# Kernel tuning notes

Hardware: AMD Instinct MI355X
Metric: run time of the kernel (lower is better)

The kernel has to match this reference:

```python
import jax, jax.numpy as jnp
import numpy as np

DIM = 1024
NUM_HEADS = 16
HEAD_DIM = DIM // NUM_HEADS
SCALE = HEAD_DIM ** -0.5


def setup_inputs() -> dict:
    key = jax.random.key(0)
    ks = jax.random.split(key, 7)
    B, N, L, C = 2, 1024, 4096, DIM
    s = C ** -0.5
    return {
        "x": jax.random.normal(ks[0], (B, N, C), jnp.float32),
        "y": jax.random.normal(ks[1], (B, L, C), jnp.float32),
        "Wq": jax.random.normal(ks[2], (C, C), jnp.float32) * s,
        "Wk": jax.random.normal(ks[3], (C, C), jnp.float32) * s,
        "Wv": jax.random.normal(ks[4], (C, C), jnp.float32) * s,
        "Wp": jax.random.normal(ks[5], (C, C), jnp.float32) * s,
        "bp": jax.random.normal(ks[6], (C,), jnp.float32) * 0.01,
    }


def reference(x, y, Wq, Wk, Wv, Wp, bp):
    B, N, C = x.shape
    L = y.shape[1]
    H, D = NUM_HEADS, HEAD_DIM
    # torch nn.Linear: out = inp @ W.T
    q = (x @ Wq.T).reshape(B, N, H, D)
    k = (y @ Wk.T).reshape(B, L, H, D)
    v = (y @ Wv.T).reshape(B, L, H, D)
    attn = jnp.einsum("bnhd,blhd->bhnl", q, k)  # [B,H,N,L]
    attn = jax.nn.softmax(SCALE * attn, axis=-1)
    out = jnp.einsum("bhnl,blhd->bnhd", attn, v).reshape(B, N, C)
    return out @ Wp.T + bp
```

## Files before the change

### kernel.cpp

```cpp
#include <hip/hip_runtime.h>
#include <hip/hip_bf16.h>
#include <stdint.h>

typedef __bf16 bf16x8 __attribute__((ext_vector_type(8)));
typedef float f32x4 __attribute__((ext_vector_type(4)));

#define MFMA16(a, b, c) __builtin_amdgcn_mfma_f32_16x16x32_bf16((a), (b), (c), 0, 0, 0)

__device__ __forceinline__ ushort f2bf(float f) {
  union { float f; uint32_t u; } a; a.f = f;
  uint32_t u = a.u;
  return (ushort)((u + 0x7fffu + ((u >> 16) & 1u)) >> 16);
}

__device__ __forceinline__ void glds16(const void* g, void* l) {
  __builtin_amdgcn_global_load_lds(
      (const __attribute__((address_space(1))) uint32_t*)g,
      (__attribute__((address_space(3))) uint32_t*)l, 16, 0, 0);
}

__global__ __launch_bounds__(256) void cvt_xy(const float* __restrict__ x,
                                              const float* __restrict__ y,
                                              ushort* __restrict__ xb,
                                              ushort* __restrict__ yb) {
  const int bid = blockIdx.x;
  const float* in;
  ushort* out;
  int i;
  if (bid < 2048) { in = x; out = xb; i = bid * 1024 + threadIdx.x * 4; }
  else            { in = y; out = yb; i = (bid - 2048) * 1024 + threadIdx.x * 4; }
  float4 v = *(const float4*)(in + i);
  ushort4 o;
  o.x = f2bf(v.x); o.y = f2bf(v.y); o.z = f2bf(v.z); o.w = f2bf(v.w);
  *(ushort4*)(out + i) = o;
}

__global__ __launch_bounds__(256) void cvt_w(
    const float* __restrict__ a, const float* __restrict__ b,
    const float* __restrict__ c, const float* __restrict__ d,
    ushort* __restrict__ oa, ushort* __restrict__ ob,
    ushort* __restrict__ oc, ushort* __restrict__ od) {
  const int bid = blockIdx.x;
  const int sel = bid >> 10;
  const int i = (bid & 1023) * 1024 + threadIdx.x * 4;
  const float* in = (sel == 0) ? a : (sel == 1) ? b : (sel == 2) ? c : d;
  ushort* out = (sel == 0) ? oa : (sel == 1) ? ob : (sel == 2) ? oc : od;
  float4 v = *(const float4*)(in + i);
  ushort4 o;
  o.x = f2bf(v.x); o.y = f2bf(v.y); o.z = f2bf(v.z); o.w = f2bf(v.w);
  *(ushort4*)(out + i) = o;
}

template <int EPI, int BM>
__global__ __launch_bounds__(256) void gemm_bt(
    const ushort* __restrict__ A, const ushort* __restrict__ Bw,
    void* __restrict__ Cout, int K, float scale, const float* __restrict__ bias) {
  constexpr int NN = 1024;
  constexpr int WM = BM / 2;
  constexpr int AM = WM / 16;
  __shared__ ushort ldsA[BM * 32];
  __shared__ ushort ldsB[128 * 32];
  __shared__ ushort ldsT[(EPI == 1) ? (4 * 64 * 64) : 8];

  const int tid = threadIdx.x;
  const int w = tid >> 6, l = tid & 63;
  const int wm = w >> 1, wn = w & 1;
  const int m0 = blockIdx.x * BM, n0 = blockIdx.y * 128;

  f32x4 acc[AM][4] = {};

  const int srow = l >> 2;
  const int schunk = l & 3;

  for (int kt = 0; kt < K; kt += 32) {
#pragma unroll
    for (int r = 0; r < BM / 64; ++r) {
      const int rb = r * 64 + w * 16;
      const int row = rb + srow;
      const int j = schunk ^ ((row >> 1) & 3);
      glds16(A + (size_t)(m0 + row) * K + kt + j * 8, (char*)ldsA + rb * 64);
    }
#pragma unroll
    for (int r = 0; r < 2; ++r) {
      const int rb = r * 64 + w * 16;
      const int row = rb + srow;
      const int j = schunk ^ ((row >> 1) & 3);
      glds16(Bw + (size_t)(n0 + row) * K + kt + j * 8, (char*)ldsB + rb * 64);
    }
    __syncthreads();
    bf16x8 af[AM], bfr[4];
#pragma unroll
    for (int t = 0; t < AM; ++t) {
      const int rt = wm * WM + t * 16 + (l & 15);
      const int j = (l >> 4) ^ ((rt >> 1) & 3);
      af[t] = *(const bf16x8*)((const char*)ldsA + rt * 64 + j * 16);
    }
#pragma unroll
    for (int t = 0; t < 4; ++t) {
      const int rt = wn * 64 + t * 16 + (l & 15);
      const int j = (l >> 4) ^ ((rt >> 1) & 3);
      bfr[t] = *(const bf16x8*)((const char*)ldsB + rt * 64 + j * 16);
    }
#pragma unroll
    for (int am = 0; am < AM; ++am)
#pragma unroll
      for (int bn = 0; bn < 4; ++bn)
        acc[am][bn] = MFMA16(af[am], bfr[bn], acc[am][bn]);
    __syncthreads();
  }

  if constexpr (EPI == 0) {
#pragma unroll
    for (int am = 0; am < AM; ++am)
#pragma unroll
      for (int bn = 0; bn < 4; ++bn)
#pragma unroll
        for (int i = 0; i < 4; ++i) {
          const int row = m0 + wm * WM + am * 16 + (l >> 4) * 4 + i;
          const int col = n0 + wn * 64 + bn * 16 + (l & 15);
          ((ushort*)Cout)[(size_t)row * NN + col] = f2bf(acc[am][bn][i] * scale);
        }
  } else if constexpr (EPI == 2) {
#pragma unroll
    for (int am = 0; am < AM; ++am)
#pragma unroll
      for (int bn = 0; bn < 4; ++bn)
#pragma unroll
        for (int i = 0; i < 4; ++i) {
          const int row = m0 + wm * WM + am * 16 + (l >> 4) * 4 + i;
          const int col = n0 + wn * 64 + bn * 16 + (l & 15);
          ((float*)Cout)[(size_t)row * NN + col] = acc[am][bn][i] + bias[col];
        }
  } else {
    ushort* tp = ldsT + w * 4096;
#pragma unroll
    for (int am = 0; am < AM; ++am)
#pragma unroll
      for (int bn = 0; bn < 4; ++bn)
#pragma unroll
        for (int i = 0; i < 4; ++i) {
          const int ml = am * 16 + (l >> 4) * 4 + i;
          const int cl = bn * 16 + (l & 15);
          tp[cl * 64 + ml] = f2bf(acc[am][bn][i]);
        }
    __syncthreads();
#pragma unroll
    for (int it = 0; it < 8; ++it) {
      const int cl = it * 8 + (l >> 3);
      const int mc = l & 7;
      bf16x8 vv = *(const bf16x8*)(tp + cl * 64 + mc * 8);
      const int gcol = n0 + wn * 64 + cl;
      const int gm = m0 + wm * WM + mc * 8;
      const int b = gm >> 12;
      const int l_ = gm & 4095;
      const int h = gcol >> 6, d = gcol & 63;
      *(bf16x8*)((ushort*)Cout + (((size_t)b * 16 + h) * 64 + d) * 4096 + l_) = vv;
    }
  }
}

__global__ __launch_bounds__(256) void attn_fused(
    const ushort* __restrict__ qb, const ushort* __restrict__ kb,
    const ushort* __restrict__ vT, ushort* __restrict__ ao) {
  constexpr int H = 16, D = 64, L = 4096, N = 1024, KB = 128;
  __shared__ ushort ldsK[2][KB * 64];
  __shared__ ushort ldsV[2][64 * KB];
  __shared__ ushort ldsP[4 * 16 * KB];

  const int tid = threadIdx.x, w = tid >> 6, l = tid & 63;
  const int wg = blockIdx.x;
  const int v = (wg & 7) * 64 + (wg >> 3);
  const int bh = v >> 4;
  const int n0 = (v & 15) * 64;
  const int b = bh >> 4, h = bh & 15;

  bf16x8 qf[2];
  {
    const int qrow = n0 + w * 16 + (l & 15);
    const ushort* qp = qb + (((size_t)b * N + qrow) * H + h) * D + (l >> 4) * 8;
    qf[0] = *(const bf16x8*)qp;
    qf[1] = *(const bf16x8*)(qp + 32);
  }

  f32x4 oacc[4] = {};
  float m_run[4], l_run[4];
#pragma unroll
  for (int i = 0; i < 4; ++i) { m_run[i] = -1e30f; l_run[i] = 0.f; }

  auto stage = [&](int buf, int l0) {
#pragma unroll
    for (int r = 0; r < 4; ++r) {
      const int rb = (w * 4 + r) * 8;
      const int row = rb + (l >> 3);
      const int j = (l & 7) ^ (row & 7);
      glds16(kb + (((size_t)b * L + l0 + row) * H + h) * D + j * 8,
             (char*)ldsK[buf] + rb * 128);
    }
#pragma unroll
    for (int r = 0; r < 4; ++r) {
      const int rb = (w * 4 + r) * 4;
      const int row = rb + (l >> 4);
      const int j = (l & 15) ^ (row & 15);
      glds16(vT + ((size_t)(b * H + h) * D + row) * L + l0 + j * 8,
             (char*)ldsV[buf] + rb * 256);
    }
  };

  stage(0, 0);

  for (int t = 0; t < L / KB; ++t) {
    const int buf = t & 1;
    if (t < L / KB - 1) {
      stage(buf ^ 1, (t + 1) * KB);
      asm volatile("s_waitcnt vmcnt(8)" ::: "memory");
    } else {
      asm volatile("s_waitcnt vmcnt(0)" ::: "memory");
    }
    __builtin_amdgcn_sched_barrier(0);
    __builtin_amdgcn_s_barrier();
    __builtin_amdgcn_sched_barrier(0);

    f32x4 sacc[8] = {};
#pragma unroll
    for (int c = 0; c < 8; ++c) {
      const int rt = c * 16 + (l & 15);
#pragma unroll
      for (int ks = 0; ks < 2; ++ks) {
        const int j = ks * 4 + (l >> 4);
        bf16x8 kf = *(const bf16x8*)((const char*)ldsK[buf] + rt * 128 + ((j ^ (rt & 7)) << 4));
        sacc[c] = MFMA16(qf[ks], kf, sacc[c]);
      }
    }

    float corr[4];
#pragma unroll
    for (int i = 0; i < 4; ++i) {
      float mt = sacc[0][i];
#pragma unroll
      for (int c = 1; c < 8; ++c) mt = fmaxf(mt, sacc[c][i]);
#pragma unroll
      for (int dd = 1; dd < 16; dd <<= 1) mt = fmaxf(mt, __shfl_xor(mt, dd, 64));
      const float mn = fmaxf(m_run[i], mt);
      corr[i] = __builtin_amdgcn_exp2f(m_run[i] - mn);
      float rs = 0.f;
#pragma unroll
      for (int c = 0; c < 8; ++c) {
        const float p = __builtin_amdgcn_exp2f(sacc[c][i] - mn);
        sacc[c][i] = p;
        rs += p;
      }
#pragma unroll
      for (int dd = 1; dd < 16; dd <<= 1) rs += __shfl_xor(rs, dd, 64);
      l_run[i] = l_run[i] * corr[i] + rs;
      m_run[i] = mn;
    }
#pragma unroll
    for (int c = 0; c < 4; ++c)
#pragma unroll
      for (int i = 0; i < 4; ++i) oacc[c][i] *= corr[i];

    ushort* pp = ldsP + w * 2048;
#pragma unroll
    for (int c = 0; c < 8; ++c)
#pragma unroll
      for (int i = 0; i < 4; ++i) {
        const int row = (l >> 4) * 4 + i;
        const int col = c * 16 + (l & 15);
        *(ushort*)((char*)pp + row * 256 + (((col >> 3) ^ row) << 4) + ((col & 7) << 1)) =
            f2bf(sacc[c][i]);
      }
    asm volatile("s_waitcnt lgkmcnt(0)" ::: "memory");
    __builtin_amdgcn_sched_barrier(0);

    bf16x8 pf[4];
#pragma unroll
    for (int ks = 0; ks < 4; ++ks) {
      const int rt = l & 15;
      const int j = ks * 4 + (l >> 4);
      pf[ks] = *(const bf16x8*)((const char*)pp + rt * 256 + ((j ^ rt) << 4));
    }
#pragma unroll
    for (int c = 0; c < 4; ++c) {
      const int rt = c * 16 + (l & 15);
#pragma unroll
      for (int ks = 0; ks < 4; ++ks) {
        const int j = ks * 4 + (l >> 4);
        bf16x8 vf = *(const bf16x8*)((const char*)ldsV[buf] + rt * 256 + ((j ^ (rt & 15)) << 4));
        oacc[c] = MFMA16(pf[ks], vf, oacc[c]);
      }
    }
    __builtin_amdgcn_sched_barrier(0);
    __builtin_amdgcn_s_barrier();
    __builtin_amdgcn_sched_barrier(0);
  }

#pragma unroll
  for (int c = 0; c < 4; ++c)
#pragma unroll
    for (int i = 0; i < 4; ++i) {
      const int n = n0 + w * 16 + (l >> 4) * 4 + i;
      const int d = c * 16 + (l & 15);
      ao[(((size_t)b * N + n) * H + h) * D + d] = f2bf(oacc[c][i] / l_run[i]);
    }
}

extern "C" void kernel_launch(void* const* d_in, const int* in_sizes, int n_in,
                              void* d_out, int out_size, void* d_ws, size_t ws_size,
                              hipStream_t stream) {
  const float* x  = (const float*)d_in[0];
  const float* y  = (const float*)d_in[1];
  const float* Wq = (const float*)d_in[2];
  const float* Wk = (const float*)d_in[3];
  const float* Wv = (const float*)d_in[4];
  const float* Wp = (const float*)d_in[5];
  const float* bp = (const float*)d_in[6];
  float* out = (float*)d_out;

  const size_t M1 = 1u << 20;
  ushort* wsb = (ushort*)d_ws;
  ushort* xb  = wsb;
  ushort* yb  = wsb + 2 * M1;
  ushort* wqb = wsb + 10 * M1;
  ushort* wkb = wsb + 11 * M1;
  ushort* wvb = wsb + 12 * M1;
  ushort* wpb = wsb + 13 * M1;
  ushort* qbf = wsb + 14 * M1;
  ushort* kbf = wsb + 16 * M1;
  ushort* vtb = wsb + 24 * M1;
  ushort* aob = wsb + 32 * M1;

  cvt_xy<<<10240, 256, 0, stream>>>(x, y, xb, yb);
  cvt_w<<<4096, 256, 0, stream>>>(Wq, Wk, Wv, Wp, wqb, wkb, wvb, wpb);

  const float qscale = 0.125f * 1.4426950408889634f;
  gemm_bt<0, 64><<<dim3(32, 8), 256, 0, stream>>>(xb, wqb, qbf, 1024, qscale, nullptr);
  gemm_bt<0, 128><<<dim3(64, 8), 256, 0, stream>>>(yb, wkb, kbf, 1024, 1.0f, nullptr);
  gemm_bt<1, 128><<<dim3(64, 8), 256, 0, stream>>>(yb, wvb, vtb, 1024, 1.0f, nullptr);

  attn_fused<<<512, 256, 0, stream>>>(qbf, kbf, vtb, aob);

  gemm_bt<2, 64><<<dim3(32, 8), 256, 0, stream>>>(aob, wpb, out, 1024, 1.0f, bp);
}
```

Before: 290.5 us.

## Keep softmax probabilities in registers, double-buffer GEMM tiles, shrink small GEMM tiles

Result: faster. 262.6 us (-9.6%).

```diff
diff --git a/kernel.cpp b/kernel.cpp
--- a/kernel.cpp
+++ b/kernel.cpp
@@ -3,9 +3,11 @@
 #include <stdint.h>
 
 typedef __bf16 bf16x8 __attribute__((ext_vector_type(8)));
+typedef __bf16 bf16x4 __attribute__((ext_vector_type(4)));
 typedef float f32x4 __attribute__((ext_vector_type(4)));
 
 #define MFMA16(a, b, c) __builtin_amdgcn_mfma_f32_16x16x32_bf16((a), (b), (c), 0, 0, 0)
+#define SB() __builtin_amdgcn_sched_barrier(0)
 
 __device__ __forceinline__ ushort f2bf(float f) {
   union { float f; uint32_t u; } a; a.f = f;
@@ -51,84 +53,96 @@
   *(ushort4*)(out + i) = o;
 }
 
-template <int EPI, int BM>
+template <int EPI, int BM, int BN>
 __global__ __launch_bounds__(256) void gemm_bt(
     const ushort* __restrict__ A, const ushort* __restrict__ Bw,
     void* __restrict__ Cout, int K, float scale, const float* __restrict__ bias) {
   constexpr int NN = 1024;
-  constexpr int WM = BM / 2;
-  constexpr int AM = WM / 16;
-  __shared__ ushort ldsA[BM * 32];
-  __shared__ ushort ldsB[128 * 32];
+  constexpr int WM = BM / 2, WN = BN / 2;
+  constexpr int AM = WM / 16, BNF = WN / 16;
+  __shared__ ushort ldsA[2][BM * 32];
+  __shared__ ushort ldsB[2][BN * 32];
   __shared__ ushort ldsT[(EPI == 1) ? (4 * 64 * 64) : 8];
 
   const int tid = threadIdx.x;
   const int w = tid >> 6, l = tid & 63;
   const int wm = w >> 1, wn = w & 1;
-  const int m0 = blockIdx.x * BM, n0 = blockIdx.y * 128;
-
-  f32x4 acc[AM][4] = {};
+  const int m0 = blockIdx.x * BM, n0 = blockIdx.y * BN;
+
+  f32x4 acc[AM][BNF] = {};
 
   const int srow = l >> 2;
   const int schunk = l & 3;
 
-  for (int kt = 0; kt < K; kt += 32) {
+  auto stage = [&](int buf, int kt) {
 #pragma unroll
     for (int r = 0; r < BM / 64; ++r) {
       const int rb = r * 64 + w * 16;
       const int row = rb + srow;
       const int j = schunk ^ ((row >> 1) & 3);
-      glds16(A + (size_t)(m0 + row) * K + kt + j * 8, (char*)ldsA + rb * 64);
-    }
-#pragma unroll
-    for (int r = 0; r < 2; ++r) {
+      glds16(A + (size_t)(m0 + row) * K + kt + j * 8, (char*)&ldsA[buf][0] + rb * 64);
+    }
+#pragma unroll
+    for (int r = 0; r < BN / 64; ++r) {
       const int rb = r * 64 + w * 16;
       const int row = rb + srow;
       const int j = schunk ^ ((row >> 1) & 3);
-      glds16(Bw + (size_t)(n0 + row) * K + kt + j * 8, (char*)ldsB + rb * 64);
-    }
-    __syncthreads();
-    bf16x8 af[AM], bfr[4];
-#pragma unroll
-    for (int t = 0; t < AM; ++t) {
-      const int rt = wm * WM + t * 16 + (l & 15);
+      glds16(Bw + (size_t)(n0 + row) * K + kt + j * 8, (char*)&ldsB[buf][0] + rb * 64);
+    }
+  };
+
+  const int nt = K / 32;
+  stage(0, 0);
+  asm volatile("s_waitcnt vmcnt(0)" ::: "memory");
+  SB(); __builtin_amdgcn_s_barrier(); SB();
+
+  for (int t = 0; t < nt; ++t) {
+    const int buf = t & 1;
+    if (t + 1 < nt) stage(buf ^ 1, (t + 1) * 32);
+    bf16x8 af[AM], bfr[BNF];
+#pragma unroll
+    for (int a = 0; a < AM; ++a) {
+      const int rt = wm * WM + a * 16 + (l & 15);
       const int j = (l >> 4) ^ ((rt >> 1) & 3);
-      af[t] = *(const bf16x8*)((const char*)ldsA + rt * 64 + j * 16);
-    }
-#pragma unroll
-    for (int t = 0; t < 4; ++t) {
-      const int rt = wn * 64 + t * 16 + (l & 15);
+      af[a] = *(const bf16x8*)((const char*)&ldsA[buf][0] + rt * 64 + j * 16);
+    }
+#pragma unroll
+    for (int bx = 0; bx < BNF; ++bx) {
+      const int rt = wn * WN + bx * 16 + (l & 15);
       const int j = (l >> 4) ^ ((rt >> 1) & 3);
-      bfr[t] = *(const bf16x8*)((const char*)ldsB + rt * 64 + j * 16);
+      bfr[bx] = *(const bf16x8*)((const char*)&ldsB[buf][0] + rt * 64 + j * 16);
     }
 #pragma unroll
     for (int am = 0; am < AM; ++am)
 #pragma unroll
-      for (int bn = 0; bn < 4; ++bn)
+      for (int bn = 0; bn < BNF; ++bn)
         acc[am][bn] = MFMA16(af[am], bfr[bn], acc[am][bn]);
-    __syncthreads();
+    if (t + 1 < nt) {
+      asm volatile("s_waitcnt vmcnt(0)" ::: "memory");
+      SB(); __builtin_amdgcn_s_barrier(); SB();
+    }
   }
 
   if constexpr (EPI == 0) {
 #pragma unroll
     for (int am = 0; am < AM; ++am)
 #pragma unroll
-      for (int bn = 0; bn < 4; ++bn)
+      for (int bn = 0; bn < BNF; ++bn)
 #pragma unroll
         for (int i = 0; i < 4; ++i) {
           const int row = m0 + wm * WM + am * 16 + (l >> 4) * 4 + i;
-          const int col = n0 + wn * 64 + bn * 16 + (l & 15);
+          const int col = n0 + wn * WN + bn * 16 + (l & 15);
           ((ushort*)Cout)[(size_t)row * NN + col] = f2bf(acc[am][bn][i] * scale);
         }
   } else if constexpr (EPI == 2) {
 #pragma unroll
     for (int am = 0; am < AM; ++am)
 #pragma unroll
-      for (int bn = 0; bn < 4; ++bn)
+      for (int bn = 0; bn < BNF; ++bn)
 #pragma unroll
         for (int i = 0; i < 4; ++i) {
           const int row = m0 + wm * WM + am * 16 + (l >> 4) * 4 + i;
-          const int col = n0 + wn * 64 + bn * 16 + (l & 15);
+          const int col = n0 + wn * WN + bn * 16 + (l & 15);
           ((float*)Cout)[(size_t)row * NN + col] = acc[am][bn][i] + bias[col];
         }
   } else {
@@ -136,7 +150,7 @@
 #pragma unroll
     for (int am = 0; am < AM; ++am)
 #pragma unroll
-      for (int bn = 0; bn < 4; ++bn)
+      for (int bn = 0; bn < BNF; ++bn)
 #pragma unroll
         for (int i = 0; i < 4; ++i) {
           const int ml = am * 16 + (l >> 4) * 4 + i;
@@ -149,7 +163,7 @@
       const int cl = it * 8 + (l >> 3);
       const int mc = l & 7;
       bf16x8 vv = *(const bf16x8*)(tp + cl * 64 + mc * 8);
-      const int gcol = n0 + wn * 64 + cl;
+      const int gcol = n0 + wn * WN + cl;
       const int gm = m0 + wm * WM + mc * 8;
       const int b = gm >> 12;
       const int l_ = gm & 4095;
@@ -165,7 +179,6 @@
   constexpr int H = 16, D = 64, L = 4096, N = 1024, KB = 128;
   __shared__ ushort ldsK[2][KB * 64];
   __shared__ ushort ldsV[2][64 * KB];
-  __shared__ ushort ldsP[4 * 16 * KB];
 
   const int tid = threadIdx.x, w = tid >> 6, l = tid & 63;
   const int wg = blockIdx.x;
@@ -173,19 +186,18 @@
   const int bh = v >> 4;
   const int n0 = (v & 15) * 64;
   const int b = bh >> 4, h = bh & 15;
+  const int hq = l >> 4;
 
   bf16x8 qf[2];
   {
     const int qrow = n0 + w * 16 + (l & 15);
-    const ushort* qp = qb + (((size_t)b * N + qrow) * H + h) * D + (l >> 4) * 8;
+    const ushort* qp = qb + (((size_t)b * N + qrow) * H + h) * D + hq * 8;
     qf[0] = *(const bf16x8*)qp;
     qf[1] = *(const bf16x8*)(qp + 32);
   }
 
   f32x4 oacc[4] = {};
-  float m_run[4], l_run[4];
-#pragma unroll
-  for (int i = 0; i < 4; ++i) { m_run[i] = -1e30f; l_run[i] = 0.f; }
+  float m_run = -1e30f, l_run = 0.f;
 
   auto stage = [&](int buf, int l0) {
 #pragma unroll
@@ -194,7 +206,7 @@
       const int row = rb + (l >> 3);
       const int j = (l & 7) ^ (row & 7);
       glds16(kb + (((size_t)b * L + l0 + row) * H + h) * D + j * 8,
-             (char*)ldsK[buf] + rb * 128);
+             (char*)&ldsK[buf][0] + rb * 128);
     }
 #pragma unroll
     for (int r = 0; r < 4; ++r) {
@@ -202,7 +214,7 @@
       const int row = rb + (l >> 4);
       const int j = (l & 15) ^ (row & 15);
       glds16(vT + ((size_t)(b * H + h) * D + row) * L + l0 + j * 8,
-             (char*)ldsV[buf] + rb * 256);
+             (char*)&ldsV[buf][0] + rb * 256);
     }
   };
 
@@ -216,9 +228,7 @@
     } else {
       asm volatile("s_waitcnt vmcnt(0)" ::: "memory");
     }
-    __builtin_amdgcn_sched_barrier(0);
-    __builtin_amdgcn_s_barrier();
-    __builtin_amdgcn_sched_barrier(0);
+    SB(); __builtin_amdgcn_s_barrier(); SB();
 
     f32x4 sacc[8] = {};
 #pragma unroll
@@ -226,81 +236,78 @@
       const int rt = c * 16 + (l & 15);
 #pragma unroll
       for (int ks = 0; ks < 2; ++ks) {
-        const int j = ks * 4 + (l >> 4);
-        bf16x8 kf = *(const bf16x8*)((const char*)ldsK[buf] + rt * 128 + ((j ^ (rt & 7)) << 4));
-        sacc[c] = MFMA16(qf[ks], kf, sacc[c]);
+        const int j = ks * 4 + hq;
+        bf16x8 kf = *(const bf16x8*)((const char*)&ldsK[buf][0] + rt * 128 + ((j ^ (rt & 7)) << 4));
+        sacc[c] = MFMA16(kf, qf[ks], sacc[c]);
       }
     }
 
-    float corr[4];
-#pragma unroll
-    for (int i = 0; i < 4; ++i) {
-      float mt = sacc[0][i];
-#pragma unroll
-      for (int c = 1; c < 8; ++c) mt = fmaxf(mt, sacc[c][i]);
-#pragma unroll
-      for (int dd = 1; dd < 16; dd <<= 1) mt = fmaxf(mt, __shfl_xor(mt, dd, 64));
-      const float mn = fmaxf(m_run[i], mt);
-      corr[i] = __builtin_amdgcn_exp2f(m_run[i] - mn);
-      float rs = 0.f;
-#pragma unroll
-      for (int c = 0; c < 8; ++c) {
+    float mt = -1e30f;
+#pragma unroll
+    for (int c = 0; c < 8; ++c)
+#pragma unroll
+      for (int i = 0; i < 4; ++i) mt = fmaxf(mt, sacc[c][i]);
+    mt = fmaxf(mt, __shfl_xor(mt, 16, 64));
+    mt = fmaxf(mt, __shfl_xor(mt, 32, 64));
+    const float mn = fmaxf(m_run, mt);
+    const float corr = __builtin_amdgcn_exp2f(m_run - mn);
+    float rs = 0.f;
+#pragma unroll
+    for (int c = 0; c < 8; ++c)
+#pragma unroll
+      for (int i = 0; i < 4; ++i) {
         const float p = __builtin_amdgcn_exp2f(sacc[c][i] - mn);
         sacc[c][i] = p;
         rs += p;
       }
-#pragma unroll
-      for (int dd = 1; dd < 16; dd <<= 1) rs += __shfl_xor(rs, dd, 64);
-      l_run[i] = l_run[i] * corr[i] + rs;
-      m_run[i] = mn;
-    }
+    rs += __shfl_xor(rs, 16, 64);
+    rs += __shfl_xor(rs, 32, 64);
+    l_run = l_run * corr + rs;
+    m_run = mn;
+
+    float corrO[4];
+#pragma unroll
+    for (int i = 0; i < 4; ++i) corrO[i] = __shfl(corr, hq * 4 + i, 64);
 #pragma unroll
     for (int c = 0; c < 4; ++c)
 #pragma unroll
-      for (int i = 0; i < 4; ++i) oacc[c][i] *= corr[i];
-
-    ushort* pp = ldsP + w * 2048;
-#pragma unroll
-    for (int c = 0; c < 8; ++c)
+      for (int i = 0; i < 4; ++i) oacc[c][i] *= corrO[i];
+
+    bf16x8 pf[4];
+#pragma unroll
+    for (int ks = 0; ks < 4; ++ks)
 #pragma unroll
       for (int i = 0; i < 4; ++i) {
-        const int row = (l >> 4) * 4 + i;
-        const int col = c * 16 + (l & 15);
-        *(ushort*)((char*)pp + row * 256 + (((col >> 3) ^ row) << 4) + ((col & 7) << 1)) =
-            f2bf(sacc[c][i]);
+        pf[ks][i]     = (__bf16)sacc[2 * ks][i];
+        pf[ks][4 + i] = (__bf16)sacc[2 * ks + 1][i];
       }
-    asm volatile("s_waitcnt lgkmcnt(0)" ::: "memory");
-    __builtin_amdgcn_sched_barrier(0);
-
-    bf16x8 pf[4];
-#pragma unroll
-    for (int ks = 0; ks < 4; ++ks) {
-      const int rt = l & 15;
-      const int j = ks * 4 + (l >> 4);
-      pf[ks] = *(const bf16x8*)((const char*)pp + rt * 256 + ((j ^ rt) << 4));
-    }
+
 #pragma unroll
     for (int c = 0; c < 4; ++c) {
       const int rt = c * 16 + (l & 15);
+      const char* vrow = (const char*)&ldsV[buf][0] + rt * 256 + ((hq & 1) << 3);
 #pragma unroll
       for (int ks = 0; ks < 4; ++ks) {
-        const int j = ks * 4 + (l >> 4);
-        bf16x8 vf = *(const bf16x8*)((const char*)ldsV[buf] + rt * 256 + ((j ^ (rt & 15)) << 4));
+        const int j0 = ks * 4 + (hq >> 1);
+        bf16x4 va = *(const bf16x4*)(vrow + ((j0 ^ (rt & 15)) << 4));
+        bf16x4 vb = *(const bf16x4*)(vrow + (((j0 + 2) ^ (rt & 15)) << 4));
+        bf16x8 vf = __builtin_shufflevector(va, vb, 0, 1, 2, 3, 4, 5, 6, 7);
         oacc[c] = MFMA16(pf[ks], vf, oacc[c]);
       }
     }
-    __builtin_amdgcn_sched_barrier(0);
-    __builtin_amdgcn_s_barrier();
-    __builtin_amdgcn_sched_barrier(0);
+    SB(); __builtin_amdgcn_s_barrier(); SB();
   }
 
+  float lr[4];
+#pragma unroll
+  for (int i = 0; i < 4; ++i) lr[i] = __shfl(l_run, hq * 4 + i, 64);
 #pragma unroll
   for (int c = 0; c < 4; ++c)
 #pragma unroll
     for (int i = 0; i < 4; ++i) {
-      const int n = n0 + w * 16 + (l >> 4) * 4 + i;
+      const int n = n0 + w * 16 + hq * 4 + i;
       const int d = c * 16 + (l & 15);
-      ao[(((size_t)b * N + n) * H + h) * D + d] = f2bf(oacc[c][i] / l_run[i]);
+      ao[(((size_t)b * N + n) * H + h) * D + d] = f2bf(oacc[c][i] / lr[i]);
     }
 }
 
@@ -333,11 +340,11 @@
   cvt_w<<<4096, 256, 0, stream>>>(Wq, Wk, Wv, Wp, wqb, wkb, wvb, wpb);
 
   const float qscale = 0.125f * 1.4426950408889634f;
-  gemm_bt<0, 64><<<dim3(32, 8), 256, 0, stream>>>(xb, wqb, qbf, 1024, qscale, nullptr);
-  gemm_bt<0, 128><<<dim3(64, 8), 256, 0, stream>>>(yb, wkb, kbf, 1024, 1.0f, nullptr);
-  gemm_bt<1, 128><<<dim3(64, 8), 256, 0, stream>>>(yb, wvb, vtb, 1024, 1.0f, nullptr);
+  gemm_bt<0, 64, 64><<<dim3(32, 16), 256, 0, stream>>>(xb, wqb, qbf, 1024, qscale, nullptr);
+  gemm_bt<0, 128, 128><<<dim3(64, 8), 256, 0, stream>>>(yb, wkb, kbf, 1024, 1.0f, nullptr);
+  gemm_bt<1, 128, 128><<<dim3(64, 8), 256, 0, stream>>>(yb, wvb, vtb, 1024, 1.0f, nullptr);
 
   attn_fused<<<512, 256, 0, stream>>>(qbf, kbf, vtb, aob);
 
-  gemm_bt<2, 64><<<dim3(32, 8), 256, 0, stream>>>(aob, wpb, out, 1024, 1.0f, bp);
-}
+  gemm_bt<2, 64, 64><<<dim3(32, 16), 256, 0, stream>>>(aob, wpb, out, 1024, 1.0f, bp);
+}
```
